# Kernel optimization log

Measured on AMD Instinct MI355X. Metric: run time of the kernel, lower is better.

Reference implementation:

```python
import jax, jax.numpy as jnp
import numpy as np

DT, TAU = 0.02, 0.1


def setup_inputs() -> dict:
    key = jax.random.key(0)
    ks = jax.random.split(key, 7)
    B, T, IN, H = 64, 2048, 64, 256
    return {
        "x0": jax.random.normal(ks[0], (B, H), jnp.float32),
        "I": jax.random.normal(ks[1], (B, T, IN), jnp.float32),
        "W_in": jax.random.normal(ks[2], (H, IN), jnp.float32) / np.sqrt(IN),
        "W_rec": jax.random.normal(ks[3], (H, H), jnp.float32) / np.sqrt(H),
        "b": jax.random.normal(ks[4], (H,), jnp.float32) * 0.1,
        "Wout": jax.random.normal(ks[5], (2, H), jnp.float32) / np.sqrt(H),
        "bout": jax.random.normal(ks[6], (2,), jnp.float32) * 0.1,
    }


def reference(x0, I, W_in, W_rec, b, Wout, bout):
    # Continuous-time leaky RNN, forward-Euler integration.
    # u_{t+1} = (1 - dt/tau) * u_t + (dt/tau) * (tanh(u_t) @ W_rec^T + I_t @ W_in^T + b)
    alpha = DT / TAU

    def step(u, I_t):
        r = jnp.tanh(u)                                   # [B, H]
        drive = r @ W_rec.T + I_t @ W_in.T + b            # [B, H]
        u_new = (1.0 - alpha) * u + alpha * drive
        return u_new, u_new

    I_tbf = jnp.swapaxes(I, 0, 1)                         # [T, B, IN]
    _, us = jax.lax.scan(step, x0, I_tbf)                 # [T, B, H]
    u = jnp.swapaxes(us, 0, 1)                            # [B, T, H]
    y = u @ Wout.T + bout                                 # [B, T, 2] linear readout
    return u, y
```

## Files before the change

kernel.cpp:

```cpp
#include <hip/hip_runtime.h>

#define BB 64
#define TT 2048
#define INW 64
#define HH 256

typedef float v2f __attribute__((ext_vector_type(2)));

__device__ __forceinline__ v2f fma2(v2f a, v2f b, v2f c) {
#if __has_builtin(__builtin_elementwise_fma)
    return __builtin_elementwise_fma(a, b, c);
#else
    v2f r; r.x = __builtin_fmaf(a.x, b.x, c.x); r.y = __builtin_fmaf(a.y, b.y, c.y); return r;
#endif
}

__device__ __forceinline__ float fast_tanh(float x) {
    float e = __expf(2.0f * x);
    return 1.0f - 2.0f / (e + 1.0f);
}

__global__ __launch_bounds__(512, 2)
void rnn_scan(const float* __restrict__ x0,
              const float* __restrict__ I,
              const float* __restrict__ W_in,
              const float* __restrict__ W_rec,
              const float* __restrict__ bias,
              float* __restrict__ u_out)
{
    __shared__ __align__(16) float r_buf[HH];
    __shared__ __align__(16) float i_buf[INW];
    __shared__ float part[4][HH + 1];

    const int b   = blockIdx.x;
    const int tid = threadIdx.x;
    const int h2  = tid & 127;
    const int q   = tid >> 7;
    const int k0  = q * 64;
    const int j0  = q * 16;
    const int hA  = h2;
    const int hB  = h2 + 128;

    v2f wrA[32], wrB[32], wiA[8], wiB[8];
    {
        const float4* wa = (const float4*)(W_rec + (size_t)hA * HH + k0);
        const float4* wb = (const float4*)(W_rec + (size_t)hB * HH + k0);
        #pragma unroll
        for (int i = 0; i < 16; ++i) {
            float4 a = wa[i], bq = wb[i];
            wrA[2*i]     = (v2f){a.x, a.y};  wrA[2*i + 1] = (v2f){a.z, a.w};
            wrB[2*i]     = (v2f){bq.x, bq.y}; wrB[2*i + 1] = (v2f){bq.z, bq.w};
        }
        const float4* ia = (const float4*)(W_in + (size_t)hA * INW + j0);
        const float4* ib = (const float4*)(W_in + (size_t)hB * INW + j0);
        #pragma unroll
        for (int i = 0; i < 4; ++i) {
            float4 a = ia[i], bq = ib[i];
            wiA[2*i]     = (v2f){a.x, a.y};  wiA[2*i + 1] = (v2f){a.z, a.w};
            wiB[2*i]     = (v2f){bq.x, bq.y}; wiB[2*i + 1] = (v2f){bq.z, bq.w};
        }
    }

    float u = 0.0f, bv = 0.0f;
    if (tid < HH) {
        u  = x0[(size_t)b * HH + tid];
        bv = bias[tid];
        r_buf[tid] = fast_tanh(u);
    }
    if (tid < INW) i_buf[tid] = I[((size_t)b * TT + 0) * INW + tid];
    __syncthreads();

    const float4* rb4 = (const float4*)&r_buf[k0];
    const float4* ib4 = (const float4*)&i_buf[j0];

    for (int t = 0; t < TT; ++t) {
        float i_next = 0.0f;
        if (tid < INW && (t + 1) < TT)
            i_next = I[((size_t)b * TT + (t + 1)) * INW + tid];

        v2f aA0 = {0.f,0.f}, aA1 = {0.f,0.f}, aB0 = {0.f,0.f}, aB1 = {0.f,0.f};
        #pragma unroll
        for (int i = 0; i < 16; ++i) {
            float4 r4 = rb4[i];
            v2f r01 = (v2f){r4.x, r4.y}, r23 = (v2f){r4.z, r4.w};
            aA0 = fma2(wrA[2*i],     r01, aA0);
            aA1 = fma2(wrA[2*i + 1], r23, aA1);
            aB0 = fma2(wrB[2*i],     r01, aB0);
            aB1 = fma2(wrB[2*i + 1], r23, aB1);
        }
        #pragma unroll
        for (int i = 0; i < 4; ++i) {
            float4 r4 = ib4[i];
            v2f r01 = (v2f){r4.x, r4.y}, r23 = (v2f){r4.z, r4.w};
            aA0 = fma2(wiA[2*i],     r01, aA0);
            aA1 = fma2(wiA[2*i + 1], r23, aA1);
            aB0 = fma2(wiB[2*i],     r01, aB0);
            aB1 = fma2(wiB[2*i + 1], r23, aB1);
        }
        v2f sA = aA0 + aA1, sB = aB0 + aB1;
        part[q][hA] = sA.x + sA.y;
        part[q][hB] = sB.x + sB.y;
        __syncthreads();

        if (tid < HH) {
            float d = ((part[0][tid] + part[1][tid]) + (part[2][tid] + part[3][tid])) + bv;
            u = 0.8f * u + 0.2f * d;
            u_out[((size_t)b * TT + t) * HH + tid] = u;
            r_buf[tid] = fast_tanh(u);
        }
        if (tid < INW) i_buf[tid] = i_next;
        __syncthreads();
    }
}

__global__ __launch_bounds__(256)
void readout(const float* __restrict__ u,
             const float* __restrict__ Wout,
             const float* __restrict__ bout,
             float* __restrict__ y)
{
    const int wid  = threadIdx.x >> 6;
    const int lane = threadIdx.x & 63;
    const size_t row = (size_t)blockIdx.x * 4 + wid;

    float4 uv = ((const float4*)(u + row * HH))[lane];
    float4 w0 = ((const float4*)Wout)[lane];
    float4 w1 = ((const float4*)(Wout + HH))[lane];

    float acc0 = uv.x * w0.x + uv.y * w0.y + uv.z * w0.z + uv.w * w0.w;
    float acc1 = uv.x * w1.x + uv.y * w1.y + uv.z * w1.z + uv.w * w1.w;

    #pragma unroll
    for (int m = 32; m >= 1; m >>= 1) {
        acc0 += __shfl_xor(acc0, m, 64);
        acc1 += __shfl_xor(acc1, m, 64);
    }
    if (lane == 0) {
        y[row * 2 + 0] = acc0 + bout[0];
        y[row * 2 + 1] = acc1 + bout[1];
    }
}

extern "C" void kernel_launch(void* const* d_in, const int* in_sizes, int n_in,
                              void* d_out, int out_size, void* d_ws, size_t ws_size,
                              hipStream_t stream) {
    const float* x0    = (const float*)d_in[0];
    const float* I     = (const float*)d_in[1];
    const float* W_in  = (const float*)d_in[2];
    const float* W_rec = (const float*)d_in[3];
    const float* bias  = (const float*)d_in[4];
    const float* Wout  = (const float*)d_in[5];
    const float* bout  = (const float*)d_in[6];

    float* u_out = (float*)d_out;
    float* y_out = u_out + (size_t)BB * TT * HH;

    rnn_scan<<<BB, 512, 0, stream>>>(x0, I, W_in, W_rec, bias, u_out);
    readout<<<(BB * TT) / 4, 256, 0, stream>>>(u_out, Wout, bout, y_out);
}
```

Baseline: 1.571 ms.

## Batch 16 sequences per block and compute recurrence with bf16 MFMA

```diff
diff --git a/kernel.cpp b/kernel.cpp
--- a/kernel.cpp
+++ b/kernel.cpp
@@ -1,115 +1,160 @@
 #include <hip/hip_runtime.h>
 
-#define BB 64
-#define TT 2048
+#define BB  64
+#define TT  2048
+#define HH  256
 #define INW 64
-#define HH 256
-
-typedef float v2f __attribute__((ext_vector_type(2)));
-
-__device__ __forceinline__ v2f fma2(v2f a, v2f b, v2f c) {
-#if __has_builtin(__builtin_elementwise_fma)
-    return __builtin_elementwise_fma(a, b, c);
-#else
-    v2f r; r.x = __builtin_fmaf(a.x, b.x, c.x); r.y = __builtin_fmaf(a.y, b.y, c.y); return r;
-#endif
-}
-
+#define BPG 16
+
+using bf16x8 = __attribute__((ext_vector_type(8))) short;
+using f32x4  = __attribute__((ext_vector_type(4))) float;
+
+__device__ __forceinline__ unsigned short f2bf(float x) {
+    unsigned int u = __float_as_uint(x);
+    return (unsigned short)((u + 0x7FFFu + ((u >> 16) & 1u)) >> 16);
+}
+__device__ __forceinline__ unsigned int packbf(float a, float b) {
+    return (unsigned int)f2bf(a) | ((unsigned int)f2bf(b) << 16);
+}
 __device__ __forceinline__ float fast_tanh(float x) {
     float e = __expf(2.0f * x);
     return 1.0f - 2.0f / (e + 1.0f);
 }
 
-__global__ __launch_bounds__(512, 2)
-void rnn_scan(const float* __restrict__ x0,
-              const float* __restrict__ I,
-              const float* __restrict__ W_in,
-              const float* __restrict__ W_rec,
-              const float* __restrict__ bias,
-              float* __restrict__ u_out)
+__global__ __launch_bounds__(256, 1)
+void rnn_scan_mfma(const float* __restrict__ x0,
+                   const float* __restrict__ I,
+                   const float* __restrict__ W_in,
+                   const float* __restrict__ W_rec,
+                   const float* __restrict__ bias,
+                   float* __restrict__ u_out)
 {
-    __shared__ __align__(16) float r_buf[HH];
-    __shared__ __align__(16) float i_buf[INW];
-    __shared__ float part[4][HH + 1];
-
-    const int b   = blockIdx.x;
-    const int tid = threadIdx.x;
-    const int h2  = tid & 127;
-    const int q   = tid >> 7;
-    const int k0  = q * 64;
-    const int j0  = q * 16;
-    const int hA  = h2;
-    const int hB  = h2 + 128;
-
-    v2f wrA[32], wrB[32], wiA[8], wiB[8];
-    {
-        const float4* wa = (const float4*)(W_rec + (size_t)hA * HH + k0);
-        const float4* wb = (const float4*)(W_rec + (size_t)hB * HH + k0);
-        #pragma unroll
-        for (int i = 0; i < 16; ++i) {
-            float4 a = wa[i], bq = wb[i];
-            wrA[2*i]     = (v2f){a.x, a.y};  wrA[2*i + 1] = (v2f){a.z, a.w};
-            wrB[2*i]     = (v2f){bq.x, bq.y}; wrB[2*i + 1] = (v2f){bq.z, bq.w};
-        }
-        const float4* ia = (const float4*)(W_in + (size_t)hA * INW + j0);
-        const float4* ib = (const float4*)(W_in + (size_t)hB * INW + j0);
-        #pragma unroll
-        for (int i = 0; i < 4; ++i) {
-            float4 a = ia[i], bq = ib[i];
-            wiA[2*i]     = (v2f){a.x, a.y};  wiA[2*i + 1] = (v2f){a.z, a.w};
-            wiB[2*i]     = (v2f){bq.x, bq.y}; wiB[2*i + 1] = (v2f){bq.z, bq.w};
-        }
-    }
-
-    float u = 0.0f, bv = 0.0f;
-    if (tid < HH) {
-        u  = x0[(size_t)b * HH + tid];
-        bv = bias[tid];
-        r_buf[tid] = fast_tanh(u);
-    }
-    if (tid < INW) i_buf[tid] = I[((size_t)b * TT + 0) * INW + tid];
+    __shared__ __align__(16) unsigned short r_lds[2][BPG][264];
+    __shared__ __align__(16) unsigned short i_lds[3][BPG][72];
+
+    const int g    = blockIdx.x;
+    const int tid  = threadIdx.x;
+    const int w    = tid >> 6;
+    const int lane = tid & 63;
+    const int c    = lane & 15;
+    const int q    = lane >> 4;
+
+    int hrow[4];
+    #pragma unroll
+    for (int tau = 0; tau < 4; ++tau)
+        hrow[tau] = w * 64 + (tau >> 1) * 32 + 2 * c + (tau & 1);
+
+    bf16x8 Brec[4][8], Bin[4][2];
+    #pragma unroll
+    for (int tau = 0; tau < 4; ++tau) {
+        const float* wr = W_rec + (size_t)hrow[tau] * HH;
+        #pragma unroll
+        for (int kk = 0; kk < 8; ++kk) {
+            bf16x8 f;
+            #pragma unroll
+            for (int j = 0; j < 8; ++j) f[j] = (short)f2bf(wr[kk * 32 + q * 8 + j]);
+            Brec[tau][kk] = f;
+        }
+        const float* wi = W_in + (size_t)hrow[tau] * INW;
+        #pragma unroll
+        for (int kk = 0; kk < 2; ++kk) {
+            bf16x8 f;
+            #pragma unroll
+            for (int j = 0; j < 8; ++j) f[j] = (short)f2bf(wi[kk * 32 + q * 8 + j]);
+            Bin[tau][kk] = f;
+        }
+    }
+
+    float bv[4];
+    #pragma unroll
+    for (int tau = 0; tau < 4; ++tau) bv[tau] = bias[hrow[tau]];
+
+    float u[4][4];
+    #pragma unroll
+    for (int tau = 0; tau < 4; ++tau)
+        #pragma unroll
+        for (int r = 0; r < 4; ++r)
+            u[tau][r] = x0[(size_t)(g * BPG + 4 * q + r) * HH + hrow[tau]];
+
+    #pragma unroll
+    for (int r = 0; r < 4; ++r) {
+        const int bb = 4 * q + r;
+        *(unsigned int*)&r_lds[0][bb][w * 64 + 2 * c] =
+            packbf(fast_tanh(u[0][r]), fast_tanh(u[1][r]));
+        *(unsigned int*)&r_lds[0][bb][w * 64 + 32 + 2 * c] =
+            packbf(fast_tanh(u[2][r]), fast_tanh(u[3][r]));
+    }
+
+    const int ib = tid >> 4;
+    const int ij = (tid & 15) * 4;
+    const float* Ib = I + (size_t)(g * BPG + ib) * TT * INW + ij;
+    #pragma unroll
+    for (int row = 0; row < 2; ++row) {
+        float4 v = *(const float4*)(Ib + (size_t)row * INW);
+        uint2 p; p.x = packbf(v.x, v.y); p.y = packbf(v.z, v.w);
+        *(uint2*)&i_lds[row][ib][ij] = p;
+    }
+    float4 iregA = *(const float4*)(Ib + (size_t)2 * INW);
+    float4 iregB;
+
     __syncthreads();
 
-    const float4* rb4 = (const float4*)&r_buf[k0];
-    const float4* ib4 = (const float4*)&i_buf[j0];
-
-    for (int t = 0; t < TT; ++t) {
-        float i_next = 0.0f;
-        if (tid < INW && (t + 1) < TT)
-            i_next = I[((size_t)b * TT + (t + 1)) * INW + tid];
-
-        v2f aA0 = {0.f,0.f}, aA1 = {0.f,0.f}, aB0 = {0.f,0.f}, aB1 = {0.f,0.f};
-        #pragma unroll
-        for (int i = 0; i < 16; ++i) {
-            float4 r4 = rb4[i];
-            v2f r01 = (v2f){r4.x, r4.y}, r23 = (v2f){r4.z, r4.w};
-            aA0 = fma2(wrA[2*i],     r01, aA0);
-            aA1 = fma2(wrA[2*i + 1], r23, aA1);
-            aB0 = fma2(wrB[2*i],     r01, aB0);
-            aB1 = fma2(wrB[2*i + 1], r23, aB1);
-        }
-        #pragma unroll
-        for (int i = 0; i < 4; ++i) {
-            float4 r4 = ib4[i];
-            v2f r01 = (v2f){r4.x, r4.y}, r23 = (v2f){r4.z, r4.w};
-            aA0 = fma2(wiA[2*i],     r01, aA0);
-            aA1 = fma2(wiA[2*i + 1], r23, aA1);
-            aB0 = fma2(wiB[2*i],     r01, aB0);
-            aB1 = fma2(wiB[2*i + 1], r23, aB1);
-        }
-        v2f sA = aA0 + aA1, sB = aB0 + aB1;
-        part[q][hA] = sA.x + sA.y;
-        part[q][hB] = sB.x + sB.y;
+    const size_t ub0 = (size_t)(g * BPG) * TT * HH;
+
+    auto step = [&](int t, float4& icur, float4& inext) {
+        int rr = t + 3; if (rr > TT - 1) rr = TT - 1;
+        inext = *(const float4*)(Ib + (size_t)rr * INW);
+
+        const int buf = t & 1;
+        f32x4 acc[4];
+        #pragma unroll
+        for (int tau = 0; tau < 4; ++tau)
+            acc[tau] = (f32x4){bv[tau], bv[tau], bv[tau], bv[tau]};
+
+        #pragma unroll
+        for (int kk = 0; kk < 8; ++kk) {
+            bf16x8 a = *(const bf16x8*)&r_lds[buf][c][kk * 32 + q * 8];
+            #pragma unroll
+            for (int tau = 0; tau < 4; ++tau)
+                acc[tau] = __builtin_amdgcn_mfma_f32_16x16x32_bf16(a, Brec[tau][kk], acc[tau], 0, 0, 0);
+        }
+        const int islot = t % 3;
+        #pragma unroll
+        for (int kk = 0; kk < 2; ++kk) {
+            bf16x8 a = *(const bf16x8*)&i_lds[islot][c][kk * 32 + q * 8];
+            #pragma unroll
+            for (int tau = 0; tau < 4; ++tau)
+                acc[tau] = __builtin_amdgcn_mfma_f32_16x16x32_bf16(a, Bin[tau][kk], acc[tau], 0, 0, 0);
+        }
+
+        #pragma unroll
+        for (int r = 0; r < 4; ++r) {
+            #pragma unroll
+            for (int tau = 0; tau < 4; ++tau)
+                u[tau][r] = 0.8f * u[tau][r] + 0.2f * acc[tau][r];
+
+            const int bb = 4 * q + r;
+            const size_t ubase = ub0 + ((size_t)bb * TT + t) * HH;
+            float2 s0 = {u[0][r], u[1][r]};
+            float2 s1 = {u[2][r], u[3][r]};
+            *(float2*)&u_out[ubase + w * 64 + 2 * c]      = s0;
+            *(float2*)&u_out[ubase + w * 64 + 32 + 2 * c] = s1;
+            *(unsigned int*)&r_lds[buf ^ 1][bb][w * 64 + 2 * c] =
+                packbf(fast_tanh(u[0][r]), fast_tanh(u[1][r]));
+            *(unsigned int*)&r_lds[buf ^ 1][bb][w * 64 + 32 + 2 * c] =
+                packbf(fast_tanh(u[2][r]), fast_tanh(u[3][r]));
+        }
+
+        {
+            uint2 p; p.x = packbf(icur.x, icur.y); p.y = packbf(icur.z, icur.w);
+            *(uint2*)&i_lds[(t + 2) % 3][ib][ij] = p;
+        }
         __syncthreads();
-
-        if (tid < HH) {
-            float d = ((part[0][tid] + part[1][tid]) + (part[2][tid] + part[3][tid])) + bv;
-            u = 0.8f * u + 0.2f * d;
-            u_out[((size_t)b * TT + t) * HH + tid] = u;
-            r_buf[tid] = fast_tanh(u);
-        }
-        if (tid < INW) i_buf[tid] = i_next;
-        __syncthreads();
+    };
+
+    for (int t = 0; t < TT; t += 2) {
+        step(t,     iregA, iregB);
+        step(t + 1, iregB, iregA);
     }
 }
 
@@ -155,6 +200,6 @@
     float* u_out = (float*)d_out;
     float* y_out = u_out + (size_t)BB * TT * HH;
 
-    rnn_scan<<<BB, 512, 0, stream>>>(x0, I, W_in, W_rec, bias, u_out);
+    rnn_scan_mfma<<<BB / BPG, 256, 0, stream>>>(x0, I, W_in, W_rec, bias, u_out);
     readout<<<(BB * TT) / 4, 256, 0, stream>>>(u_out, Wout, bout, y_out);
 }
```

New measurement: 2.887 ms. +83.7%, slower.
